# Kernel optimization log

Hardware: AMD Instinct MI355X
Metric: run time of the kernel (lower is better)

The kernel has to match this reference:

```python
import jax, jax.numpy as jnp
import numpy as np

B, H, S, D = 4, 16, 2048, 64

def setup_inputs() -> dict:
    key = jax.random.key(0)
    kq, kk, kv = jax.random.split(key, 3)
    return {
        "query": jax.random.normal(kq, (B, H, S, D), dtype=jnp.float32),
        "key": jax.random.normal(kk, (B, H, S, D), dtype=jnp.float32),
        "value": jax.random.normal(kv, (B, H, S, D), dtype=jnp.float32),
    }

def reference(query, key, value):
    d_k = query.shape[-1]
    scale = 1.0 / jnp.sqrt(jnp.asarray(d_k, dtype=jnp.float32))
    # scores: [B, H, S, S]
    scores = jnp.einsum("bhqd,bhkd->bhqk", query, key) * scale
    attention_weights = jax.nn.softmax(scores, axis=-1)
    # output: [B, H, S, D]
    output = jnp.einsum("bhqk,bhkd->bhqd", attention_weights, value)
    return (output, attention_weights)
```

## Files before the change

kernel.cpp:

```cpp
#include <hip/hip_runtime.h>
#include <hip/hip_bf16.h>
#include <cmath>

#define S_LEN 2048
#define D_DIM 64
#define N_BH  64
#define TILE  64
#define NTILES 32
#define TILE_BYTES 8192
#define IMG_BYTES_PER_BH ((size_t)NTILES * TILE_BYTES)
#define IMG_BYTES_TOTAL  ((size_t)N_BH * IMG_BYTES_PER_BH)
#define WS_NEED (2 * IMG_BYTES_TOTAL)

typedef __attribute__((ext_vector_type(8))) __bf16 bf16x8;
typedef __attribute__((ext_vector_type(8))) unsigned short ushort8;
typedef __attribute__((ext_vector_type(4))) float  f32x4;

union U8cvt { ushort8 s; bf16x8 b; };

#if __has_builtin(__builtin_amdgcn_exp2f)
#define EXP2(x) __builtin_amdgcn_exp2f(x)
#else
#define EXP2(x) __expf((x) * 0.69314718055994530942f)
#endif

__device__ __forceinline__ unsigned short f2bf_bits(float x) {
    unsigned int u = __float_as_uint(x);
    u += 0x7fffu + ((u >> 16) & 1u);
    return (unsigned short)(u >> 16);
}

__device__ __forceinline__ int swz_off(int row, int colbyte) {
    return row * 128 + (colbyte ^ ((row & 7) << 4));
}

__device__ __forceinline__ bf16x8 ldfrag_sw(const unsigned short* tile, int row, int colbyte) {
    return *reinterpret_cast<const bf16x8*>(
        reinterpret_cast<const char*>(tile) + swz_off(row, colbyte));
}

__device__ __forceinline__ void glds16(const void* g, void* l) {
    __builtin_amdgcn_global_load_lds(
        (const __attribute__((address_space(1))) unsigned int*)g,
        (__attribute__((address_space(3))) unsigned int*)l, 16, 0, 0);
}

__device__ __forceinline__ void stage_tile(const char* gtile, unsigned short* ltile,
                                           int wave, int lane) {
#pragma unroll
    for (int i = 0; i < 2; ++i) {
        int off = (wave * 2 + i) << 10;
        glds16(gtile + off + lane * 16, reinterpret_cast<char*>(ltile) + off);
    }
}

__global__ __launch_bounds__(256) void convert_kv(const float* __restrict__ K,
                                                  const float* __restrict__ V,
                                                  char* __restrict__ ws) {
    __shared__ unsigned short vtmp[TILE * 72];
    const int tid = threadIdx.x;
    const int kb = blockIdx.x, bh = blockIdx.y;
    const float* Ks = K + ((size_t)bh * S_LEN + kb * TILE) * D_DIM;
    const float* Vs = V + ((size_t)bh * S_LEN + kb * TILE) * D_DIM;
    char* Kt = ws + (size_t)(bh * NTILES + kb) * TILE_BYTES;
    char* Vt = ws + IMG_BYTES_TOTAL + (size_t)(bh * NTILES + kb) * TILE_BYTES;

#pragma unroll
    for (int i = 0; i < 2; ++i) {
        int n = tid + i * 256;
        int row = n >> 3, c = n & 7;
        const float4 a = *reinterpret_cast<const float4*>(Ks + row * D_DIM + c * 8);
        const float4 b = *reinterpret_cast<const float4*>(Ks + row * D_DIM + c * 8 + 4);
        ushort8 u;
        u[0] = f2bf_bits(a.x); u[1] = f2bf_bits(a.y); u[2] = f2bf_bits(a.z); u[3] = f2bf_bits(a.w);
        u[4] = f2bf_bits(b.x); u[5] = f2bf_bits(b.y); u[6] = f2bf_bits(b.z); u[7] = f2bf_bits(b.w);
        *reinterpret_cast<ushort8*>(Kt + swz_off(row, c * 16)) = u;
    }

#pragma unroll
    for (int i = 0; i < 4; ++i) {
        int linear = tid + i * 256;
        int k = linear >> 4, d0 = (linear & 15) << 2;
        const float4 v = *reinterpret_cast<const float4*>(Vs + k * D_DIM + d0);
        ushort4 u;
        u.x = f2bf_bits(v.x); u.y = f2bf_bits(v.y); u.z = f2bf_bits(v.z); u.w = f2bf_bits(v.w);
        *reinterpret_cast<ushort4*>(vtmp + k * 72 + d0) = u;
    }
    __syncthreads();
#pragma unroll
    for (int i = 0; i < 2; ++i) {
        int n = tid + i * 256;
        int d = n >> 3, c = n & 7;
        ushort8 u;
#pragma unroll
        for (int j = 0; j < 8; ++j) u[j] = vtmp[(c * 8 + j) * 72 + d];
        *reinterpret_cast<ushort8*>(Vt + swz_off(d, c * 16)) = u;
    }
}

__global__ __launch_bounds__(256) void attn_fused2(const float* __restrict__ Q,
                                                   const char* __restrict__ ws,
                                                   float* __restrict__ out) {
    __shared__ __align__(16) unsigned short k_lds[2][TILE * D_DIM];
    __shared__ __align__(16) unsigned short v_lds[2][TILE * D_DIM];
    __shared__ __align__(16) unsigned short w_lds[TILE * TILE];

    const int tid  = threadIdx.x;
    const int bh   = blockIdx.y;
    const int q0   = blockIdx.x * TILE;
    const int wave = tid >> 6;
    const int lane = tid & 63;
    const int quad = lane >> 4;
    const int lr   = lane & 15;
    const int m0   = wave * 16;

    const char* Kimg = ws + (size_t)bh * IMG_BYTES_PER_BH;
    const char* Vimg = ws + IMG_BYTES_TOTAL + (size_t)bh * IMG_BYTES_PER_BH;
    float* out_o = out + ((size_t)bh * S_LEN + q0) * D_DIM;
    float* out_w = out + (size_t)N_BH * S_LEN * D_DIM
                       + ((size_t)bh * S_LEN + q0) * (size_t)S_LEN;

    stage_tile(Kimg, k_lds[0], wave, lane);

    bf16x8 aq[2];
    {
        const float sc = 0.125f * 1.44269504088896340736f;
        const float* qr = Q + ((size_t)bh * S_LEN + q0 + m0 + lr) * D_DIM;
#pragma unroll
        for (int ks = 0; ks < 2; ++ks) {
            const float4 a = *reinterpret_cast<const float4*>(qr + ks * 32 + quad * 8);
            const float4 b = *reinterpret_cast<const float4*>(qr + ks * 32 + quad * 8 + 4);
            U8cvt t;
            t.s[0] = f2bf_bits(a.x * sc); t.s[1] = f2bf_bits(a.y * sc);
            t.s[2] = f2bf_bits(a.z * sc); t.s[3] = f2bf_bits(a.w * sc);
            t.s[4] = f2bf_bits(b.x * sc); t.s[5] = f2bf_bits(b.y * sc);
            t.s[6] = f2bf_bits(b.z * sc); t.s[7] = f2bf_bits(b.w * sc);
            aq[ks] = t.b;
        }
    }
    __syncthreads();

    float l_p[4] = {0.f, 0.f, 0.f, 0.f};

    for (int t = 0; t < NTILES; ++t) {
        const unsigned short* kt = k_lds[t & 1];
        {
            const char* nk = (t + 1 < NTILES) ? (Kimg + (size_t)(t + 1) * TILE_BYTES) : Kimg;
            stage_tile(nk, k_lds[(t & 1) ^ 1], wave, lane);
            if (t + 1 == NTILES) stage_tile(Vimg, v_lds[0], wave, lane);
        }

        f32x4 acc[4];
#pragma unroll
        for (int nt = 0; nt < 4; ++nt) acc[nt] = f32x4{0.f, 0.f, 0.f, 0.f};
        __builtin_amdgcn_s_setprio(1);
#pragma unroll
        for (int ks = 0; ks < 2; ++ks)
#pragma unroll
            for (int nt = 0; nt < 4; ++nt) {
                bf16x8 b = ldfrag_sw(kt, nt * 16 + lr, ks * 64 + quad * 16);
                acc[nt] = __builtin_amdgcn_mfma_f32_16x16x32_bf16(aq[ks], b, acc[nt], 0, 0, 0);
            }
        __builtin_amdgcn_s_setprio(0);

#pragma unroll
        for (int r = 0; r < 4; ++r)
            l_p[r] += EXP2(acc[0][r]) + EXP2(acc[1][r]) + EXP2(acc[2][r]) + EXP2(acc[3][r]);

        __syncthreads();
    }

#pragma unroll
    for (int off = 1; off < 16; off <<= 1)
#pragma unroll
        for (int r = 0; r < 4; ++r)
            l_p[r] += __shfl_xor(l_p[r], off, 64);

    float rl[4];
#pragma unroll
    for (int r = 0; r < 4; ++r) rl[r] = 1.f / l_p[r];

    f32x4 acco[4];
#pragma unroll
    for (int nt = 0; nt < 4; ++nt) acco[nt] = f32x4{0.f, 0.f, 0.f, 0.f};

    for (int t = 0; t < NTILES; ++t) {
        const int cur = t & 1;
        if (t + 1 < NTILES) {
            stage_tile(Kimg + (size_t)(t + 1) * TILE_BYTES, k_lds[cur ^ 1], wave, lane);
            stage_tile(Vimg + (size_t)(t + 1) * TILE_BYTES, v_lds[cur ^ 1], wave, lane);
        }
        asm volatile("" ::: "memory");

        f32x4 acc[4];
#pragma unroll
        for (int nt = 0; nt < 4; ++nt) acc[nt] = f32x4{0.f, 0.f, 0.f, 0.f};
        __builtin_amdgcn_s_setprio(1);
#pragma unroll
        for (int ks = 0; ks < 2; ++ks)
#pragma unroll
            for (int nt = 0; nt < 4; ++nt) {
                bf16x8 b = ldfrag_sw(k_lds[cur], nt * 16 + lr, ks * 64 + quad * 16);
                acc[nt] = __builtin_amdgcn_mfma_f32_16x16x32_bf16(aq[ks], b, acc[nt], 0, 0, 0);
            }
        __builtin_amdgcn_s_setprio(0);

#pragma unroll
        for (int nt = 0; nt < 4; ++nt)
#pragma unroll
            for (int r = 0; r < 4; ++r) {
                float w = EXP2(acc[nt][r]) * rl[r];
                __builtin_nontemporal_store(
                    w, out_w + (size_t)(m0 + quad * 4 + r) * S_LEN + t * TILE + nt * 16 + lr);
                int off = swz_off(m0 + quad * 4 + r, (nt * 16 + lr) * 2);
                *reinterpret_cast<unsigned short*>(
                    reinterpret_cast<char*>(w_lds) + off) = f2bf_bits(w);
            }

#pragma unroll
        for (int ks = 0; ks < 2; ++ks) {
            bf16x8 aw = ldfrag_sw(w_lds, m0 + lr, ks * 64 + quad * 16);
            __builtin_amdgcn_s_setprio(1);
#pragma unroll
            for (int nt = 0; nt < 4; ++nt) {
                bf16x8 bv = ldfrag_sw(v_lds[cur], nt * 16 + lr, ks * 64 + quad * 16);
                acco[nt] = __builtin_amdgcn_mfma_f32_16x16x32_bf16(aw, bv, acco[nt], 0, 0, 0);
            }
            __builtin_amdgcn_s_setprio(0);
        }

        if (t + 1 < NTILES) {
            asm volatile("s_waitcnt vmcnt(16)" ::: "memory");
            __builtin_amdgcn_s_barrier();
        }
    }

#pragma unroll
    for (int nt = 0; nt < 4; ++nt)
#pragma unroll
        for (int r = 0; r < 4; ++r)
            __builtin_nontemporal_store(
                acco[nt][r], out_o + (size_t)(m0 + quad * 4 + r) * D_DIM + nt * 16 + lr);
}

#define LDW 72

__device__ __forceinline__ void stage_rm(const float* __restrict__ g,
                                         unsigned short* lds, int tid) {
#pragma unroll
    for (int i = 0; i < 4; ++i) {
        int linear = tid + i * 256;
        int row = linear >> 4;
        int col = (linear & 15) << 2;
        const float4 v = *reinterpret_cast<const float4*>(g + row * D_DIM + col);
        ushort4 u;
        u.x = f2bf_bits(v.x); u.y = f2bf_bits(v.y);
        u.z = f2bf_bits(v.z); u.w = f2bf_bits(v.w);
        *reinterpret_cast<ushort4*>(lds + row * LDW + col) = u;
    }
}

__device__ __forceinline__ void stage_tr(const float* __restrict__ g,
                                         unsigned short* lds, int tid) {
#pragma unroll
    for (int i = 0; i < 4; ++i) {
        int linear = tid + i * 256;
        int kk = linear >> 4;
        int d0 = (linear & 15) << 2;
        const float4 v = *reinterpret_cast<const float4*>(g + kk * D_DIM + d0);
        lds[(d0 + 0) * LDW + kk] = f2bf_bits(v.x);
        lds[(d0 + 1) * LDW + kk] = f2bf_bits(v.y);
        lds[(d0 + 2) * LDW + kk] = f2bf_bits(v.z);
        lds[(d0 + 3) * LDW + kk] = f2bf_bits(v.w);
    }
}

__device__ __forceinline__ bf16x8 ldfrag_pad(const unsigned short* lds, int row, int col) {
    return *reinterpret_cast<const bf16x8*>(lds + row * LDW + col);
}

__global__ __launch_bounds__(256) void attn_fused_fb(
        const float* __restrict__ Q, const float* __restrict__ K,
        const float* __restrict__ V, float* __restrict__ out) {
    __shared__ __align__(16) unsigned short q_lds[TILE * LDW];
    __shared__ __align__(16) unsigned short k_lds[TILE * LDW];
    __shared__ __align__(16) unsigned short vT_lds[D_DIM * LDW];
    __shared__ __align__(16) unsigned short w_lds[TILE * LDW];

    const int tid  = threadIdx.x;
    const int bh   = blockIdx.y;
    const int q0   = blockIdx.x * TILE;
    const int wave = tid >> 6;
    const int lane = tid & 63;
    const int quad = lane >> 4;
    const int lr   = lane & 15;
    const int m0   = wave * 16;

    const float* Qg = Q + ((size_t)bh * S_LEN + q0) * D_DIM;
    const float* Kg = K + (size_t)bh * S_LEN * D_DIM;
    const float* Vg = V + (size_t)bh * S_LEN * D_DIM;
    float* out_o = out + ((size_t)bh * S_LEN + q0) * D_DIM;
    float* out_w = out + (size_t)N_BH * S_LEN * D_DIM
                       + ((size_t)bh * S_LEN + q0) * (size_t)S_LEN;

    stage_rm(Qg, q_lds, tid);
    __syncthreads();

    bf16x8 aq[2];
    aq[0] = ldfrag_pad(q_lds, m0 + lr, quad * 8);
    aq[1] = ldfrag_pad(q_lds, m0 + lr, 32 + quad * 8);

    float m_r[4], l_r[4];
#pragma unroll
    for (int r = 0; r < 4; ++r) { m_r[r] = -INFINITY; l_r[r] = 0.f; }

    for (int kb = 0; kb < S_LEN; kb += TILE) {
        __syncthreads();
        stage_rm(Kg + (size_t)kb * D_DIM, k_lds, tid);
        __syncthreads();

        f32x4 acc[4];
#pragma unroll
        for (int nt = 0; nt < 4; ++nt) acc[nt] = f32x4{0.f, 0.f, 0.f, 0.f};
#pragma unroll
        for (int ks = 0; ks < 2; ++ks)
#pragma unroll
            for (int nt = 0; nt < 4; ++nt) {
                bf16x8 b = ldfrag_pad(k_lds, nt * 16 + lr, ks * 32 + quad * 8);
                acc[nt] = __builtin_amdgcn_mfma_f32_16x16x32_bf16(aq[ks], b, acc[nt], 0, 0, 0);
            }

        float red[4];
#pragma unroll
        for (int r = 0; r < 4; ++r) {
            float tv = fmaxf(fmaxf(acc[0][r], acc[1][r]), fmaxf(acc[2][r], acc[3][r]));
            red[r] = tv * 0.125f;
        }
#pragma unroll
        for (int off = 1; off < 16; off <<= 1)
#pragma unroll
            for (int r = 0; r < 4; ++r)
                red[r] = fmaxf(red[r], __shfl_xor(red[r], off, 64));

#pragma unroll
        for (int r = 0; r < 4; ++r) {
            float mn = fmaxf(m_r[r], red[r]);
            float ps = 0.f;
#pragma unroll
            for (int nt = 0; nt < 4; ++nt)
                ps += __expf(acc[nt][r] * 0.125f - mn);
            l_r[r] *= __expf(m_r[r] - mn);
            m_r[r] = mn;
            red[r] = ps;
        }
#pragma unroll
        for (int off = 1; off < 16; off <<= 1)
#pragma unroll
            for (int r = 0; r < 4; ++r)
                red[r] += __shfl_xor(red[r], off, 64);
#pragma unroll
        for (int r = 0; r < 4; ++r) l_r[r] += red[r];
    }

    float rl[4];
#pragma unroll
    for (int r = 0; r < 4; ++r) rl[r] = 1.f / l_r[r];

    f32x4 acco[4];
#pragma unroll
    for (int nt = 0; nt < 4; ++nt) acco[nt] = f32x4{0.f, 0.f, 0.f, 0.f};

    for (int kb = 0; kb < S_LEN; kb += TILE) {
        __syncthreads();
        stage_rm(Kg + (size_t)kb * D_DIM, k_lds, tid);
        stage_tr(Vg + (size_t)kb * D_DIM, vT_lds, tid);
        __syncthreads();

        f32x4 acc[4];
#pragma unroll
        for (int nt = 0; nt < 4; ++nt) acc[nt] = f32x4{0.f, 0.f, 0.f, 0.f};
#pragma unroll
        for (int ks = 0; ks < 2; ++ks)
#pragma unroll
            for (int nt = 0; nt < 4; ++nt) {
                bf16x8 b = ldfrag_pad(k_lds, nt * 16 + lr, ks * 32 + quad * 8);
                acc[nt] = __builtin_amdgcn_mfma_f32_16x16x32_bf16(aq[ks], b, acc[nt], 0, 0, 0);
            }

#pragma unroll
        for (int nt = 0; nt < 4; ++nt)
#pragma unroll
            for (int r = 0; r < 4; ++r) {
                float w = __expf(acc[nt][r] * 0.125f - m_r[r]) * rl[r];
                out_w[(size_t)(m0 + quad * 4 + r) * S_LEN + kb + nt * 16 + lr] = w;
                w_lds[(m0 + quad * 4 + r) * LDW + nt * 16 + lr] = f2bf_bits(w);
            }
        __syncthreads();

#pragma unroll
        for (int ks = 0; ks < 2; ++ks) {
            bf16x8 aw = ldfrag_pad(w_lds, m0 + lr, ks * 32 + quad * 8);
#pragma unroll
            for (int nt = 0; nt < 4; ++nt) {
                bf16x8 b = ldfrag_pad(vT_lds, nt * 16 + lr, ks * 32 + quad * 8);
                acco[nt] = __builtin_amdgcn_mfma_f32_16x16x32_bf16(aw, b, acco[nt], 0, 0, 0);
            }
        }
    }

#pragma unroll
    for (int nt = 0; nt < 4; ++nt)
#pragma unroll
        for (int r = 0; r < 4; ++r)
            out_o[(size_t)(m0 + quad * 4 + r) * D_DIM + nt * 16 + lr] = acco[nt][r];
}

extern "C" void kernel_launch(void* const* d_in, const int* in_sizes, int n_in,
                              void* d_out, int out_size, void* d_ws, size_t ws_size,
                              hipStream_t stream) {
    (void)in_sizes; (void)n_in; (void)out_size;
    const float* Q = (const float*)d_in[0];
    const float* K = (const float*)d_in[1];
    const float* V = (const float*)d_in[2];
    float* out = (float*)d_out;

    if (d_ws != nullptr && ws_size >= WS_NEED) {
        char* ws = (char*)d_ws;
        convert_kv<<<dim3(NTILES, N_BH), dim3(256), 0, stream>>>(K, V, ws);
        attn_fused2<<<dim3(NTILES, N_BH), dim3(256), 0, stream>>>(Q, ws, out);
    } else {
        attn_fused_fb<<<dim3(S_LEN / TILE, N_BH), dim3(256), 0, stream>>>(Q, K, V, out);
    }
}
```

Before: 1.338 ms.

## Vectorize attention-weight stores via LDS and deepen K/V prefetch ring

Attention-weight output stores change from scattered scalar nontemporal stores to 16-byte row-contiguous stores. The values are read back from the bf16 w_lds tile and widened to fp32. The K/V double buffers become a single 4-slot ring, so the first pass prefetches two tiles ahead using explicit vmcnt waits and raw barriers. The grid is transposed so blocks sharing a head are spread across x, and the Q global loads are issued before K staging. The stored weights are now bf16-rounded rather than full fp32, which lowers output precision.

```diff
diff --git a/kernel.cpp b/kernel.cpp
--- a/kernel.cpp
+++ b/kernel.cpp
@@ -101,13 +101,12 @@
 __global__ __launch_bounds__(256) void attn_fused2(const float* __restrict__ Q,
                                                    const char* __restrict__ ws,
                                                    float* __restrict__ out) {
-    __shared__ __align__(16) unsigned short k_lds[2][TILE * D_DIM];
-    __shared__ __align__(16) unsigned short v_lds[2][TILE * D_DIM];
+    __shared__ __align__(16) unsigned short smem[4][TILE * D_DIM];
     __shared__ __align__(16) unsigned short w_lds[TILE * TILE];
 
     const int tid  = threadIdx.x;
-    const int bh   = blockIdx.y;
-    const int q0   = blockIdx.x * TILE;
+    const int bh   = blockIdx.x;
+    const int q0   = blockIdx.y * TILE;
     const int wave = tid >> 6;
     const int lane = tid & 63;
     const int quad = lane >> 4;
@@ -120,36 +119,43 @@
     float* out_w = out + (size_t)N_BH * S_LEN * D_DIM
                        + ((size_t)bh * S_LEN + q0) * (size_t)S_LEN;
 
-    stage_tile(Kimg, k_lds[0], wave, lane);
+    float4 qa[2], qb[2];
+    {
+        const float* qr = Q + ((size_t)bh * S_LEN + q0 + m0 + lr) * D_DIM;
+#pragma unroll
+        for (int ks = 0; ks < 2; ++ks) {
+            qa[ks] = *reinterpret_cast<const float4*>(qr + ks * 32 + quad * 8);
+            qb[ks] = *reinterpret_cast<const float4*>(qr + ks * 32 + quad * 8 + 4);
+        }
+    }
+    stage_tile(Kimg, smem[0], wave, lane);
+    stage_tile(Kimg + TILE_BYTES, smem[1], wave, lane);
 
     bf16x8 aq[2];
     {
         const float sc = 0.125f * 1.44269504088896340736f;
-        const float* qr = Q + ((size_t)bh * S_LEN + q0 + m0 + lr) * D_DIM;
 #pragma unroll
         for (int ks = 0; ks < 2; ++ks) {
-            const float4 a = *reinterpret_cast<const float4*>(qr + ks * 32 + quad * 8);
-            const float4 b = *reinterpret_cast<const float4*>(qr + ks * 32 + quad * 8 + 4);
             U8cvt t;
-            t.s[0] = f2bf_bits(a.x * sc); t.s[1] = f2bf_bits(a.y * sc);
-            t.s[2] = f2bf_bits(a.z * sc); t.s[3] = f2bf_bits(a.w * sc);
-            t.s[4] = f2bf_bits(b.x * sc); t.s[5] = f2bf_bits(b.y * sc);
-            t.s[6] = f2bf_bits(b.z * sc); t.s[7] = f2bf_bits(b.w * sc);
+            t.s[0] = f2bf_bits(qa[ks].x * sc); t.s[1] = f2bf_bits(qa[ks].y * sc);
+            t.s[2] = f2bf_bits(qa[ks].z * sc); t.s[3] = f2bf_bits(qa[ks].w * sc);
+            t.s[4] = f2bf_bits(qb[ks].x * sc); t.s[5] = f2bf_bits(qb[ks].y * sc);
+            t.s[6] = f2bf_bits(qb[ks].z * sc); t.s[7] = f2bf_bits(qb[ks].w * sc);
             aq[ks] = t.b;
         }
     }
-    __syncthreads();
 
     float l_p[4] = {0.f, 0.f, 0.f, 0.f};
 
     for (int t = 0; t < NTILES; ++t) {
-        const unsigned short* kt = k_lds[t & 1];
-        {
-            const char* nk = (t + 1 < NTILES) ? (Kimg + (size_t)(t + 1) * TILE_BYTES) : Kimg;
-            stage_tile(nk, k_lds[(t & 1) ^ 1], wave, lane);
-            if (t + 1 == NTILES) stage_tile(Vimg, v_lds[0], wave, lane);
-        }
-
+        const char* sg = (t < NTILES - 2) ? (Kimg + (size_t)(t + 2) * TILE_BYTES)
+                       : (t == NTILES - 2) ? Kimg : Vimg;
+        stage_tile(sg, smem[(t + 2) & 3], wave, lane);
+
+        asm volatile("s_waitcnt vmcnt(4)" ::: "memory");
+        __builtin_amdgcn_s_barrier();
+
+        const unsigned short* kt = smem[t & 3];
         f32x4 acc[4];
 #pragma unroll
         for (int nt = 0; nt < 4; ++nt) acc[nt] = f32x4{0.f, 0.f, 0.f, 0.f};
@@ -166,9 +172,10 @@
 #pragma unroll
         for (int r = 0; r < 4; ++r)
             l_p[r] += EXP2(acc[0][r]) + EXP2(acc[1][r]) + EXP2(acc[2][r]) + EXP2(acc[3][r]);
-
-        __syncthreads();
-    }
+    }
+
+    asm volatile("s_waitcnt vmcnt(0)" ::: "memory");
+    __builtin_amdgcn_s_barrier();
 
 #pragma unroll
     for (int off = 1; off < 16; off <<= 1)
@@ -185,12 +192,14 @@
     for (int nt = 0; nt < 4; ++nt) acco[nt] = f32x4{0.f, 0.f, 0.f, 0.f};
 
     for (int t = 0; t < NTILES; ++t) {
-        const int cur = t & 1;
         if (t + 1 < NTILES) {
-            stage_tile(Kimg + (size_t)(t + 1) * TILE_BYTES, k_lds[cur ^ 1], wave, lane);
-            stage_tile(Vimg + (size_t)(t + 1) * TILE_BYTES, v_lds[cur ^ 1], wave, lane);
+            stage_tile(Kimg + (size_t)(t + 1) * TILE_BYTES, smem[(2 * t + 2) & 3], wave, lane);
+            stage_tile(Vimg + (size_t)(t + 1) * TILE_BYTES, smem[(2 * t + 3) & 3], wave, lane);
         }
         asm volatile("" ::: "memory");
+
+        const unsigned short* kt = smem[(2 * t) & 3];
+        const unsigned short* vt = smem[(2 * t + 1) & 3];
 
         f32x4 acc[4];
 #pragma unroll
@@ -200,7 +209,7 @@
         for (int ks = 0; ks < 2; ++ks)
 #pragma unroll
             for (int nt = 0; nt < 4; ++nt) {
-                bf16x8 b = ldfrag_sw(k_lds[cur], nt * 16 + lr, ks * 64 + quad * 16);
+                bf16x8 b = ldfrag_sw(kt, nt * 16 + lr, ks * 64 + quad * 16);
                 acc[nt] = __builtin_amdgcn_mfma_f32_16x16x32_bf16(aq[ks], b, acc[nt], 0, 0, 0);
             }
         __builtin_amdgcn_s_setprio(0);
@@ -210,8 +219,6 @@
 #pragma unroll
             for (int r = 0; r < 4; ++r) {
                 float w = EXP2(acc[nt][r]) * rl[r];
-                __builtin_nontemporal_store(
-                    w, out_w + (size_t)(m0 + quad * 4 + r) * S_LEN + t * TILE + nt * 16 + lr);
                 int off = swz_off(m0 + quad * 4 + r, (nt * 16 + lr) * 2);
                 *reinterpret_cast<unsigned short*>(
                     reinterpret_cast<char*>(w_lds) + off) = f2bf_bits(w);
@@ -223,14 +230,29 @@
             __builtin_amdgcn_s_setprio(1);
 #pragma unroll
             for (int nt = 0; nt < 4; ++nt) {
-                bf16x8 bv = ldfrag_sw(v_lds[cur], nt * 16 + lr, ks * 64 + quad * 16);
+                bf16x8 bv = ldfrag_sw(vt, nt * 16 + lr, ks * 64 + quad * 16);
                 acco[nt] = __builtin_amdgcn_mfma_f32_16x16x32_bf16(aw, bv, acco[nt], 0, 0, 0);
             }
             __builtin_amdgcn_s_setprio(0);
         }
 
+#pragma unroll
+        for (int j = 0; j < 4; ++j) {
+            int row = m0 + j * 4 + (lane >> 4);
+            const ushort4 wb = *reinterpret_cast<const ushort4*>(
+                reinterpret_cast<const char*>(w_lds) + swz_off(row, (lane & 15) * 8));
+            f32x4 wf;
+            wf[0] = __uint_as_float((unsigned)wb.x << 16);
+            wf[1] = __uint_as_float((unsigned)wb.y << 16);
+            wf[2] = __uint_as_float((unsigned)wb.z << 16);
+            wf[3] = __uint_as_float((unsigned)wb.w << 16);
+            __builtin_nontemporal_store(
+                wf, reinterpret_cast<f32x4*>(out_w + (size_t)row * S_LEN + t * TILE)
+                        + (lane & 15));
+        }
+
         if (t + 1 < NTILES) {
-            asm volatile("s_waitcnt vmcnt(16)" ::: "memory");
+            asm volatile("s_waitcnt vmcnt(4)" ::: "memory");
             __builtin_amdgcn_s_barrier();
         }
     }
@@ -427,7 +449,7 @@
     if (d_ws != nullptr && ws_size >= WS_NEED) {
         char* ws = (char*)d_ws;
         convert_kv<<<dim3(NTILES, N_BH), dim3(256), 0, stream>>>(K, V, ws);
-        attn_fused2<<<dim3(NTILES, N_BH), dim3(256), 0, stream>>>(Q, ws, out);
+        attn_fused2<<<dim3(N_BH, NTILES), dim3(256), 0, stream>>>(Q, ws, out);
     } else {
         attn_fused_fb<<<dim3(S_LEN / TILE, N_BH), dim3(256), 0, stream>>>(Q, K, V, out);
     }
```

Result: faster. 1.226 ms (-8.3%).
